# Performance work log

Hardware: AMD Instinct MI355X
Metric: run time of the kernel (lower is better)

## Reference

```python
import jax, jax.numpy as jnp
import numpy as np

B, D_IN, D_HID, D_OUT = 32768, 512, 1024, 2048

def setup_inputs() -> dict:
    key = jax.random.key(0)
    k1, k2, k3, k4 = jax.random.split(key, 4)
    x = jax.random.normal(k1, (B, D_IN), dtype=jnp.float32)
    # linear1 params (torch Linear default-style init, scale approximated)
    l1_w = jax.random.normal(k2, (D_HID, D_IN), dtype=jnp.float32) * (D_IN ** -0.5)
    l1_b = jax.random.normal(k3, (D_HID,), dtype=jnp.float32) * 0.01
    # second linear params: normal(0, hidden^-0.5) weight, zero bias as in source
    weight = jax.random.normal(k4, (D_OUT, D_HID), dtype=jnp.float32) * (D_HID ** -0.5)
    bias = jnp.zeros((D_OUT,), dtype=jnp.float32)
    return {"x": x, "l1_w": l1_w, "l1_b": l1_b, "weight": weight, "bias": bias}

def reference(x, l1_w, l1_b, weight, bias):
    # linear1: [B, D_IN] -> [B, D_HID]
    h = jnp.einsum('bi,hi->bh', x, l1_w) + l1_b
    # fused linear + max epilogue: scores [B, D_OUT] -> max over output dim
    scores = jnp.einsum('bh,oh->bo', h, weight) + bias
    return jnp.max(scores, axis=-1)  # [B]
```

## Files before the change

### kernel.cpp

```cpp
#include <hip/hip_runtime.h>
#include <hip/hip_bf16.h>
#include <stdint.h>

static constexpr int BATCH = 32768;
static constexpr int DIN   = 512;
static constexpr int DHID  = 1024;
static constexpr int DOUT  = 2048;

typedef __bf16 bf16x8 __attribute__((ext_vector_type(8)));
typedef float  f32x4  __attribute__((ext_vector_type(4)));

__device__ __forceinline__ unsigned short f2bf(float f) {
    unsigned int u = __float_as_uint(f);
    u += 0x7FFFu + ((u >> 16) & 1u);
    return (unsigned short)(u >> 16);
}

__device__ __forceinline__ void gload_lds16(const void* g, void* l) {
    __builtin_amdgcn_global_load_lds((__attribute__((address_space(1))) void*)g,
                                     (__attribute__((address_space(3))) void*)l,
                                     16, 0, 0);
}


__global__ __launch_bounds__(256) void prep_kernel(
    const float* __restrict__ w1, const float4* __restrict__ w2f,
    const float4* __restrict__ xf, const float* __restrict__ b1,
    const float* __restrict__ b2,
    unsigned short* __restrict__ w1t, ushort4* __restrict__ w2b,
    ushort4* __restrict__ xb, float* __restrict__ bp) {
    const int blk = blockIdx.x;
    const int t   = threadIdx.x;
    if (blk < 512) {
        __shared__ float tile[32][33];
        const int tileI = blk & 15;
        const int tileH = blk >> 4;
        const int iBase = tileI * 32, hBase = tileH * 32;
        const int col = t & 31, rowq = t >> 5;
#pragma unroll
        for (int p = 0; p < 4; ++p) {
            const int row = p * 8 + rowq;
            tile[row][col] = w1[(size_t)(hBase + row) * DIN + iBase + col];
        }
        __syncthreads();
#pragma unroll
        for (int p = 0; p < 4; ++p) {
            const int row = p * 8 + rowq;
            w1t[(size_t)(iBase + row) * DHID + hBase + col] = f2bf(tile[col][row]);
        }
    } else if (blk < 2560) {
        __shared__ float wsum[4];
        const int o = blk - 512;
        const size_t g = (size_t)o * 256 + t;
        float4 v = w2f[g];
        ushort4 ob;
        ob.x = f2bf(v.x); ob.y = f2bf(v.y); ob.z = f2bf(v.z); ob.w = f2bf(v.w);
        w2b[g] = ob;
        float4 bv = ((const float4*)b1)[t];
        float s = v.x * bv.x + v.y * bv.y + v.z * bv.z + v.w * bv.w;
#pragma unroll
        for (int off = 1; off < 64; off <<= 1) s += __shfl_xor(s, off);
        if ((t & 63) == 0) wsum[t >> 6] = s;
        __syncthreads();
        if (t == 0) bp[o] = wsum[0] + wsum[1] + wsum[2] + wsum[3] + b2[o];
    } else {
        const size_t base = (size_t)(blk - 2560) * 1024 + t;
#pragma unroll
        for (int i = 0; i < 4; ++i) {
            float4 v = xf[base + i * 256];
            ushort4 o;
            o.x = f2bf(v.x); o.y = f2bf(v.y); o.z = f2bf(v.z); o.w = f2bf(v.w);
            xb[base + i * 256] = o;
        }
    }
}

__global__ __launch_bounds__(256) void gemmW_kernel(
    const unsigned short* __restrict__ A,
    const unsigned short* __restrict__ Bw,
    unsigned short* __restrict__ W) {
    constexpr int K = DHID;
    __shared__ __align__(16) unsigned short sA[64 * 128];
    __shared__ __align__(16) unsigned short sB[64 * 128];

    const int tid  = threadIdx.x;
    const int lane = tid & 63;
    const int wid  = tid >> 6;
    const int wr = wid >> 1, wc = wid & 1;
    const int r = lane & 15, q = lane >> 4;
    const int blockN = blockIdx.x * 64;
    const int blockM = blockIdx.y * 64;

    const int chKey = (tid & 15) ^ ((tid >> 4) & 15);
    const size_t aBase = (size_t)(blockM + (tid >> 4)) * K + chKey * 8;
    const size_t bBase = (size_t)(blockN + (tid >> 4)) * K + chKey * 8;

    f32x4 acc[2][2];
#pragma unroll
    for (int mt = 0; mt < 2; ++mt)
#pragma unroll
        for (int nt = 0; nt < 2; ++nt) { f32x4 z = {0.f, 0.f, 0.f, 0.f}; acc[mt][nt] = z; }

    for (int k0 = 0; k0 < K; k0 += 128) {
#pragma unroll
        for (int j = 0; j < 4; ++j) {
            gload_lds16(A  + aBase + (size_t)j * 16 * K + k0, sA + j * 2048 + wid * 512);
            gload_lds16(Bw + bBase + (size_t)j * 16 * K + k0, sB + j * 2048 + wid * 512);
        }
        __syncthreads();
#pragma unroll
        for (int ks = 0; ks < 4; ++ks) {
            const int ch = ((ks << 2) + q) ^ r;
            bf16x8 af[2], bf[2];
#pragma unroll
            for (int mt = 0; mt < 2; ++mt) af[mt] = *(const bf16x8*)&sA[(wr * 32 + mt * 16 + r) * 128 + ch * 8];
#pragma unroll
            for (int nt = 0; nt < 2; ++nt) bf[nt] = *(const bf16x8*)&sB[(wc * 32 + nt * 16 + r) * 128 + ch * 8];
#pragma unroll
            for (int mt = 0; mt < 2; ++mt)
#pragma unroll
                for (int nt = 0; nt < 2; ++nt)
                    acc[mt][nt] = __builtin_amdgcn_mfma_f32_16x16x32_bf16(af[mt], bf[nt], acc[mt][nt], 0, 0, 0);
        }
        __syncthreads();
    }

#pragma unroll
    for (int mt = 0; mt < 2; ++mt) {
        const int row0 = blockM + wr * 32 + mt * 16 + q * 4;
#pragma unroll
        for (int nt = 0; nt < 2; ++nt) {
            const int col = blockN + wc * 32 + nt * 16 + r;
#pragma unroll
            for (int reg = 0; reg < 4; ++reg)
                W[(size_t)(row0 + reg) * DIN + col] = f2bf(acc[mt][nt][reg]);
        }
    }
}

__global__ __launch_bounds__(256, 2) void gemmS_kernel(
    const unsigned short* __restrict__ A,
    const unsigned short* __restrict__ Bw,
    const float* __restrict__ bp,
    float* __restrict__ out) {
    constexpr int K = DIN;
    __shared__ __align__(16) unsigned short lds[40960];

    const int tid  = threadIdx.x;
    const int lane = tid & 63;
    const int wid  = tid >> 6;
    const int r    = lane & 15, q = lane >> 4;

    const int b    = blockIdx.x;
    const int xcd  = b & 7;
    const int j    = b >> 3;
    const int blockM = (xcd * 64 + j) * 64;

    const int sRow = tid >> 2;
    const int swz  = (tid & 3) ^ ((tid >> 3) & 3);
    const unsigned short* aSrc = A  + (size_t)(blockM + sRow) * K + swz * 8;
    const unsigned short* bSrc = Bw + (size_t)sRow * K + swz * 8;

#define STAGE_A(reg, kt) \
    gload_lds16(aSrc + (kt) * 32, lds + (reg) * 2048 + wid * 512)
#define STAGE_B(bT, reg, kt) do {                                               \
    gload_lds16((bT) + (size_t)(0 * 64) * K + (kt) * 32,                        \
                lds + 8192 + (reg) * 8192 + 0 * 2048 + wid * 512);              \
    gload_lds16((bT) + (size_t)(1 * 64) * K + (kt) * 32,                        \
                lds + 8192 + (reg) * 8192 + 1 * 2048 + wid * 512);              \
    gload_lds16((bT) + (size_t)(2 * 64) * K + (kt) * 32,                        \
                lds + 8192 + (reg) * 8192 + 2 * 2048 + wid * 512);              \
    gload_lds16((bT) + (size_t)(3 * 64) * K + (kt) * 32,                        \
                lds + 8192 + (reg) * 8192 + 3 * 2048 + wid * 512);              \
} while (0)

    const int fOff = (q ^ ((r >> 1) & 3)) * 8;
    const unsigned short* ldsAf = lds + r * 32 + fOff;
    const unsigned short* ldsBf = lds + 8192 + (wid * 64 + r) * 32 + fOff;

    f32x4 acc[4][4];
#pragma unroll
    for (int mt = 0; mt < 4; ++mt)
#pragma unroll
        for (int nt = 0; nt < 4; ++nt) { f32x4 z = {0.f, 0.f, 0.f, 0.f}; acc[mt][nt] = z; }
    float mx[4][4];
#pragma unroll
    for (int mt = 0; mt < 4; ++mt)
#pragma unroll
        for (int rg = 0; rg < 4; ++rg) mx[mt][rg] = -INFINITY;
    bf16x8 af[4], bfr[4];
    float bvc[4], bvn[4];

#define RD(reg) do {                                                            \
    const unsigned short* pa_ = ldsAf + (reg) * 2048;                           \
    af[0] = *(const bf16x8*)(pa_);                                              \
    af[1] = *(const bf16x8*)(pa_ + 512);                                        \
    af[2] = *(const bf16x8*)(pa_ + 1024);                                       \
    af[3] = *(const bf16x8*)(pa_ + 1536);                                       \
    const unsigned short* pb_ = ldsBf + (reg) * 8192;                           \
    bfr[0] = *(const bf16x8*)(pb_);                                             \
    bfr[1] = *(const bf16x8*)(pb_ + 512);                                       \
    bfr[2] = *(const bf16x8*)(pb_ + 1024);                                      \
    bfr[3] = *(const bf16x8*)(pb_ + 1536);                                      \
} while (0)
#define MM() do {                                                               \
    __builtin_amdgcn_s_setprio(1);                                              \
    _Pragma("unroll") for (int m_ = 0; m_ < 4; ++m_)                            \
    _Pragma("unroll") for (int n_ = 0; n_ < 4; ++n_)                            \
        acc[m_][n_] = __builtin_amdgcn_mfma_f32_16x16x32_bf16(                  \
            af[m_], bfr[n_], acc[m_][n_], 0, 0, 0);                             \
    __builtin_amdgcn_s_setprio(0);                                              \
} while (0)
#define BAR()   __builtin_amdgcn_s_barrier()
#define LGKM0() asm volatile("s_waitcnt lgkmcnt(0)" ::: "memory")
#define VMC(n)  asm volatile("s_waitcnt vmcnt(" #n ")" ::: "memory")

#define PH(reg, sreg, skt, bT) do {                                             \
    RD(reg);                                                                    \
    STAGE_A(sreg, skt); STAGE_B(bT, sreg, skt);                                 \
    VMC(10); LGKM0(); MM(); BAR();                                              \
} while (0)
#define PH15(reg, sreg, skt, bT, bOff) do {                                     \
    RD(reg);                                                                    \
    bvn[0] = bp[(bOff) + wid * 64 + 0 * 16 + r];                                \
    bvn[1] = bp[(bOff) + wid * 64 + 1 * 16 + r];                                \
    bvn[2] = bp[(bOff) + wid * 64 + 2 * 16 + r];                                \
    bvn[3] = bp[(bOff) + wid * 64 + 3 * 16 + r];                                \
    __builtin_amdgcn_sched_barrier(0);                                          \
    STAGE_A(sreg, skt); STAGE_B(bT, sreg, skt);                                 \
    VMC(10); LGKM0(); MM(); BAR();                                              \
} while (0)

#define FOLD() do {                                                             \
    _Pragma("unroll") for (int mt_ = 0; mt_ < 4; ++mt_)                         \
    _Pragma("unroll") for (int rg_ = 0; rg_ < 4; ++rg_) {                       \
        float v_ = fmaxf(fmaxf(acc[mt_][0][rg_] + bvc[0],                       \
                               acc[mt_][1][rg_] + bvc[1]),                      \
                         fmaxf(acc[mt_][2][rg_] + bvc[2],                       \
                               acc[mt_][3][rg_] + bvc[3]));                     \
        mx[mt_][rg_] = fmaxf(mx[mt_][rg_], v_);                                 \
    }                                                                           \
} while (0)
#define ACC_ZERO() do {                                                         \
    _Pragma("unroll") for (int mt_ = 0; mt_ < 4; ++mt_)                         \
    _Pragma("unroll") for (int nt_ = 0; nt_ < 4; ++nt_) {                       \
        f32x4 z_ = {0.f, 0.f, 0.f, 0.f}; acc[mt_][nt_] = z_;                    \
    }                                                                           \
} while (0)

#pragma unroll
    for (int nt = 0; nt < 4; ++nt) bvc[nt] = bp[wid * 64 + nt * 16 + r];
    VMC(0);

    STAGE_A(0, 0); STAGE_B(bSrc, 0, 0);
    STAGE_A(1, 1); STAGE_B(bSrc, 1, 1);
    STAGE_A(2, 2); STAGE_B(bSrc, 2, 2);
    VMC(10);
    BAR();

#pragma unroll 1
    for (int t = 0; t < 7; ++t) {
        const unsigned short* bT  = bSrc + (size_t)t * 256 * K;
        const unsigned short* bTn = bT + (size_t)256 * K;
        PH(0, 3, 3, bT);
        PH(1, 0, 4, bT);
        PH(2, 1, 5, bT);
        PH(3, 2, 6, bT);
        PH(0, 3, 7, bT);
        PH(1, 0, 8, bT);
        PH(2, 1, 9, bT);
        PH(3, 2, 10, bT);
        PH(0, 3, 11, bT);
        PH(1, 0, 12, bT);
        PH(2, 1, 13, bT);
        PH(3, 2, 14, bT);
        PH(0, 3, 15, bT);
        PH(1, 0, 0, bTn);
        PH(2, 1, 1, bTn);
        PH15(3, 2, 2, bTn, (t + 1) * 256);
        FOLD();
        ACC_ZERO();
#pragma unroll
        for (int nt = 0; nt < 4; ++nt) bvc[nt] = bvn[nt];
    }
    {
        const unsigned short* bT = bSrc + (size_t)7 * 256 * K;
        PH(0, 3, 3, bT);
        PH(1, 0, 4, bT);
        PH(2, 1, 5, bT);
        PH(3, 2, 6, bT);
        PH(0, 3, 7, bT);
        PH(1, 0, 8, bT);
        PH(2, 1, 9, bT);
        PH(3, 2, 10, bT);
        PH(0, 3, 11, bT);
        PH(1, 0, 12, bT);
        PH(2, 1, 13, bT);
        PH(3, 2, 14, bT);
        PH(0, 3, 15, bT);
        RD(1); VMC(5); LGKM0(); MM(); BAR();
        RD(2); VMC(0); LGKM0(); MM(); BAR();
        RD(3); LGKM0(); MM();
        FOLD();
    }

#undef STAGE_A
#undef STAGE_B
#undef RD
#undef MM
#undef BAR
#undef LGKM0
#undef VMC
#undef PH
#undef PH15
#undef FOLD
#undef ACC_ZERO

    __syncthreads();
    float* smax = (float*)lds;
#pragma unroll
    for (int mt = 0; mt < 4; ++mt) {
#pragma unroll
        for (int rg = 0; rg < 4; ++rg) {
            float v = mx[mt][rg];
#pragma unroll
            for (int off = 1; off < 16; off <<= 1)
                v = fmaxf(v, __shfl_xor(v, off));
            if (r == 0) smax[(mt * 16 + q * 4 + rg) * 4 + wid] = v;
        }
    }
    __syncthreads();
    if (tid < 64) {
        const float* p = smax + tid * 4;
        out[blockM + tid] = fmaxf(fmaxf(p[0], p[1]), fmaxf(p[2], p[3]));
    }
}

extern "C" void kernel_launch(void* const* d_in, const int* in_sizes, int n_in,
                              void* d_out, int out_size, void* d_ws, size_t ws_size,
                              hipStream_t stream) {
    const float* x   = (const float*)d_in[0];
    const float* l1w = (const float*)d_in[1];
    const float* l1b = (const float*)d_in[2];
    const float* w2  = (const float*)d_in[3];
    const float* b2  = (const float*)d_in[4];
    float* out = (float*)d_out;

    char* ws = (char*)d_ws;
    unsigned short* w1t = (unsigned short*)(ws);
    unsigned short* w2b = (unsigned short*)(ws + 1048576);
    unsigned short* Wb  = (unsigned short*)(ws + 5242880);
    float* bp           = (float*)(ws + 7340032);
    unsigned short* xb  = (unsigned short*)(ws + 7348224);

    prep_kernel<<<6656, 256, 0, stream>>>(
        l1w, (const float4*)w2, (const float4*)x, l1b, b2,
        w1t, (ushort4*)w2b, (ushort4*)xb, bp);

    gemmW_kernel<<<dim3(DIN / 64, DOUT / 64), 256, 0, stream>>>(w2b, w1t, Wb);

    gemmS_kernel<<<512, 256, 0, stream>>>(xb, Wb, bp, out);
}
```

Baseline: 203.0 us.

## Keep full A row-block resident in LDS and stream B fragments directly from global

The main GEMM+max kernel now uses 512-thread blocks covering 128 rows, split across 2x4 waves. The whole K=512 slice of A (128x512 bf16) is staged into LDS once, and B fragments are loaded straight from global/L2 into registers with even/odd double buffering. After the first 256-column tile this removes the per-step LDS staging of B and the per-phase barriers. The cost is a large LDS footprint (~136KB) that limits occupancy to one block per CU, plus B reads that depend on L2 latency being hidden by register prefetch.

New measurement: 239.6 us. +18.0%, slower.

```diff
diff --git a/kernel.cpp b/kernel.cpp
--- a/kernel.cpp
+++ b/kernel.cpp
@@ -138,45 +138,40 @@
     }
 }
 
-__global__ __launch_bounds__(256, 2) void gemmS_kernel(
+__global__ __launch_bounds__(512, 2) void gemmS_kernel(
     const unsigned short* __restrict__ A,
     const unsigned short* __restrict__ Bw,
     const float* __restrict__ bp,
     float* __restrict__ out) {
-    constexpr int K = DIN;
-    __shared__ __align__(16) unsigned short lds[40960];
+    __shared__ __align__(16) unsigned short lds[69632];
 
     const int tid  = threadIdx.x;
     const int lane = tid & 63;
     const int wid  = tid >> 6;
+    const int wr   = wid >> 2;
+    const int wc   = wid & 3;
     const int r    = lane & 15, q = lane >> 4;
 
     const int b    = blockIdx.x;
     const int xcd  = b & 7;
     const int j    = b >> 3;
-    const int blockM = (xcd * 64 + j) * 64;
+    const int blockM = (xcd * 32 + j) * 128;
 
     const int sRow = tid >> 2;
     const int swz  = (tid & 3) ^ ((tid >> 3) & 3);
-    const unsigned short* aSrc = A  + (size_t)(blockM + sRow) * K + swz * 8;
-    const unsigned short* bSrc = Bw + (size_t)sRow * K + swz * 8;
-
-#define STAGE_A(reg, kt) \
-    gload_lds16(aSrc + (kt) * 32, lds + (reg) * 2048 + wid * 512)
-#define STAGE_B(bT, reg, kt) do {                                               \
-    gload_lds16((bT) + (size_t)(0 * 64) * K + (kt) * 32,                        \
-                lds + 8192 + (reg) * 8192 + 0 * 2048 + wid * 512);              \
-    gload_lds16((bT) + (size_t)(1 * 64) * K + (kt) * 32,                        \
-                lds + 8192 + (reg) * 8192 + 1 * 2048 + wid * 512);              \
-    gload_lds16((bT) + (size_t)(2 * 64) * K + (kt) * 32,                        \
-                lds + 8192 + (reg) * 8192 + 2 * 2048 + wid * 512);              \
-    gload_lds16((bT) + (size_t)(3 * 64) * K + (kt) * 32,                        \
-                lds + 8192 + (reg) * 8192 + 3 * 2048 + wid * 512);              \
-} while (0)
+    const unsigned short* aSrc = A + (size_t)(blockM + sRow) * DIN + swz * 8;
+    float* biasLds = (float*)(lds + 65536);
+
+#define STAGE_A(s) \
+    gload_lds16(aSrc + (s) * 32, lds + (s) * 4096 + wid * 512)
 
     const int fOff = (q ^ ((r >> 1) & 3)) * 8;
-    const unsigned short* ldsAf = lds + r * 32 + fOff;
-    const unsigned short* ldsBf = lds + 8192 + (wid * 64 + r) * 32 + fOff;
+    const unsigned short* ldsAf = lds + (wr * 64 + r) * 32 + fOff;
+
+    const unsigned short* bT0 = Bw + (size_t)(wc * 64 + 0 * 16 + r) * DIN + q * 8;
+    const unsigned short* bT1 = Bw + (size_t)(wc * 64 + 1 * 16 + r) * DIN + q * 8;
+    const unsigned short* bT2 = Bw + (size_t)(wc * 64 + 2 * 16 + r) * DIN + q * 8;
+    const unsigned short* bT3 = Bw + (size_t)(wc * 64 + 3 * 16 + r) * DIN + q * 8;
 
     f32x4 acc[4][4];
 #pragma unroll
@@ -188,48 +183,48 @@
     for (int mt = 0; mt < 4; ++mt)
 #pragma unroll
         for (int rg = 0; rg < 4; ++rg) mx[mt][rg] = -INFINITY;
-    bf16x8 af[4], bfr[4];
-    float bvc[4], bvn[4];
-
-#define RD(reg) do {                                                            \
-    const unsigned short* pa_ = ldsAf + (reg) * 2048;                           \
+    bf16x8 af[4], bfrE[4], bfrO[4];
+    float bvc[4];
+
+#define RD_A(s) do {                                                            \
+    const unsigned short* pa_ = ldsAf + (s) * 4096;                             \
     af[0] = *(const bf16x8*)(pa_);                                              \
     af[1] = *(const bf16x8*)(pa_ + 512);                                        \
     af[2] = *(const bf16x8*)(pa_ + 1024);                                       \
     af[3] = *(const bf16x8*)(pa_ + 1536);                                       \
-    const unsigned short* pb_ = ldsBf + (reg) * 8192;                           \
-    bfr[0] = *(const bf16x8*)(pb_);                                             \
-    bfr[1] = *(const bf16x8*)(pb_ + 512);                                       \
-    bfr[2] = *(const bf16x8*)(pb_ + 1024);                                      \
-    bfr[3] = *(const bf16x8*)(pb_ + 1536);                                      \
-} while (0)
-#define MM() do {                                                               \
+} while (0)
+#define BPREF_E(soff) do {                                                      \
+    bfrE[0] = *(const bf16x8*)(bT0 + (soff));                                   \
+    bfrE[1] = *(const bf16x8*)(bT1 + (soff));                                   \
+    bfrE[2] = *(const bf16x8*)(bT2 + (soff));                                   \
+    bfrE[3] = *(const bf16x8*)(bT3 + (soff));                                   \
+} while (0)
+#define BPREF_O(soff) do {                                                      \
+    bfrO[0] = *(const bf16x8*)(bT0 + (soff));                                   \
+    bfrO[1] = *(const bf16x8*)(bT1 + (soff));                                   \
+    bfrO[2] = *(const bf16x8*)(bT2 + (soff));                                   \
+    bfrO[3] = *(const bf16x8*)(bT3 + (soff));                                   \
+} while (0)
+#define MM_E() do {                                                             \
     __builtin_amdgcn_s_setprio(1);                                              \
     _Pragma("unroll") for (int m_ = 0; m_ < 4; ++m_)                            \
     _Pragma("unroll") for (int n_ = 0; n_ < 4; ++n_)                            \
         acc[m_][n_] = __builtin_amdgcn_mfma_f32_16x16x32_bf16(                  \
-            af[m_], bfr[n_], acc[m_][n_], 0, 0, 0);                             \
+            af[m_], bfrE[n_], acc[m_][n_], 0, 0, 0);                            \
     __builtin_amdgcn_s_setprio(0);                                              \
 } while (0)
+#define MM_O() do {                                                             \
+    __builtin_amdgcn_s_setprio(1);                                              \
+    _Pragma("unroll") for (int m_ = 0; m_ < 4; ++m_)                            \
+    _Pragma("unroll") for (int n_ = 0; n_ < 4; ++n_)                            \
+        acc[m_][n_] = __builtin_amdgcn_mfma_f32_16x16x32_bf16(                  \
+            af[m_], bfrO[n_], acc[m_][n_], 0, 0, 0);                            \
+    __builtin_amdgcn_s_setprio(0);                                              \
+} while (0)
 #define BAR()   __builtin_amdgcn_s_barrier()
+#define SB0()   __builtin_amdgcn_sched_barrier(0)
 #define LGKM0() asm volatile("s_waitcnt lgkmcnt(0)" ::: "memory")
 #define VMC(n)  asm volatile("s_waitcnt vmcnt(" #n ")" ::: "memory")
-
-#define PH(reg, sreg, skt, bT) do {                                             \
-    RD(reg);                                                                    \
-    STAGE_A(sreg, skt); STAGE_B(bT, sreg, skt);                                 \
-    VMC(10); LGKM0(); MM(); BAR();                                              \
-} while (0)
-#define PH15(reg, sreg, skt, bT, bOff) do {                                     \
-    RD(reg);                                                                    \
-    bvn[0] = bp[(bOff) + wid * 64 + 0 * 16 + r];                                \
-    bvn[1] = bp[(bOff) + wid * 64 + 1 * 16 + r];                                \
-    bvn[2] = bp[(bOff) + wid * 64 + 2 * 16 + r];                                \
-    bvn[3] = bp[(bOff) + wid * 64 + 3 * 16 + r];                                \
-    __builtin_amdgcn_sched_barrier(0);                                          \
-    STAGE_A(sreg, skt); STAGE_B(bT, sreg, skt);                                 \
-    VMC(10); LGKM0(); MM(); BAR();                                              \
-} while (0)
 
 #define FOLD() do {                                                             \
     _Pragma("unroll") for (int mt_ = 0; mt_ < 4; ++mt_)                         \
@@ -248,71 +243,103 @@
     }                                                                           \
 } while (0)
 
-#pragma unroll
-    for (int nt = 0; nt < 4; ++nt) bvc[nt] = bp[wid * 64 + nt * 16 + r];
-    VMC(0);
-
-    STAGE_A(0, 0); STAGE_B(bSrc, 0, 0);
-    STAGE_A(1, 1); STAGE_B(bSrc, 1, 1);
-    STAGE_A(2, 2); STAGE_B(bSrc, 2, 2);
-    VMC(10);
+    {
+        float4 bb = ((const float4*)bp)[tid];
+        ((float4*)biasLds)[tid] = bb;
+    }
+    LGKM0();
+
+    BPREF_E(0);
+    STAGE_A(0); STAGE_A(1); STAGE_A(2);
+    VMC(2);
     BAR();
 
+#pragma unroll
+    for (int nt = 0; nt < 4; ++nt) bvc[nt] = biasLds[wc * 64 + nt * 16 + r];
+
+#define PH0S(s, PREF, MM_) do {                                                 \
+    RD_A(s); PREF((s + 1) * 32); STAGE_A((s) + 3);                              \
+    VMC(6); LGKM0(); SB0(); MM_(); BAR();                                       \
+} while (0)
+    PH0S(0,  BPREF_O, MM_E);
+    PH0S(1,  BPREF_E, MM_O);
+    PH0S(2,  BPREF_O, MM_E);
+    PH0S(3,  BPREF_E, MM_O);
+    PH0S(4,  BPREF_O, MM_E);
+    PH0S(5,  BPREF_E, MM_O);
+    PH0S(6,  BPREF_O, MM_E);
+    PH0S(7,  BPREF_E, MM_O);
+    PH0S(8,  BPREF_O, MM_E);
+    PH0S(9,  BPREF_E, MM_O);
+    PH0S(10, BPREF_O, MM_E);
+    PH0S(11, BPREF_E, MM_O);
+    PH0S(12, BPREF_O, MM_E);
+    RD_A(13); BPREF_E(14 * 32); VMC(4); LGKM0(); SB0(); MM_O(); BAR();
+    RD_A(14); BPREF_O(15 * 32); VMC(4); LGKM0(); SB0(); MM_E(); BAR();
+    RD_A(15); BPREF_E(131072); VMC(4); LGKM0(); SB0(); MM_O(); BAR();
+    FOLD(); ACC_ZERO();
+#pragma unroll
+    for (int nt = 0; nt < 4; ++nt) bvc[nt] = biasLds[256 + wc * 64 + nt * 16 + r];
+    bT0 += 131072; bT1 += 131072; bT2 += 131072; bT3 += 131072;
+#undef PH0S
+
+#define PHS(s, PREF, MM_) do {                                                  \
+    RD_A(s); PREF((s + 1) * 32);                                                \
+    VMC(4); LGKM0(); SB0(); MM_();                                              \
+} while (0)
 #pragma unroll 1
-    for (int t = 0; t < 7; ++t) {
-        const unsigned short* bT  = bSrc + (size_t)t * 256 * K;
-        const unsigned short* bTn = bT + (size_t)256 * K;
-        PH(0, 3, 3, bT);
-        PH(1, 0, 4, bT);
-        PH(2, 1, 5, bT);
-        PH(3, 2, 6, bT);
-        PH(0, 3, 7, bT);
-        PH(1, 0, 8, bT);
-        PH(2, 1, 9, bT);
-        PH(3, 2, 10, bT);
-        PH(0, 3, 11, bT);
-        PH(1, 0, 12, bT);
-        PH(2, 1, 13, bT);
-        PH(3, 2, 14, bT);
-        PH(0, 3, 15, bT);
-        PH(1, 0, 0, bTn);
-        PH(2, 1, 1, bTn);
-        PH15(3, 2, 2, bTn, (t + 1) * 256);
-        FOLD();
-        ACC_ZERO();
-#pragma unroll
-        for (int nt = 0; nt < 4; ++nt) bvc[nt] = bvn[nt];
-    }
-    {
-        const unsigned short* bT = bSrc + (size_t)7 * 256 * K;
-        PH(0, 3, 3, bT);
-        PH(1, 0, 4, bT);
-        PH(2, 1, 5, bT);
-        PH(3, 2, 6, bT);
-        PH(0, 3, 7, bT);
-        PH(1, 0, 8, bT);
-        PH(2, 1, 9, bT);
-        PH(3, 2, 10, bT);
-        PH(0, 3, 11, bT);
-        PH(1, 0, 12, bT);
-        PH(2, 1, 13, bT);
-        PH(3, 2, 14, bT);
-        PH(0, 3, 15, bT);
-        RD(1); VMC(5); LGKM0(); MM(); BAR();
-        RD(2); VMC(0); LGKM0(); MM(); BAR();
-        RD(3); LGKM0(); MM();
-        FOLD();
-    }
+    for (int t = 1; t < 7; ++t) {
+        PHS(0,  BPREF_O, MM_E);
+        PHS(1,  BPREF_E, MM_O);
+        PHS(2,  BPREF_O, MM_E);
+        PHS(3,  BPREF_E, MM_O);
+        PHS(4,  BPREF_O, MM_E);
+        PHS(5,  BPREF_E, MM_O);
+        PHS(6,  BPREF_O, MM_E);
+        PHS(7,  BPREF_E, MM_O);
+        PHS(8,  BPREF_O, MM_E);
+        PHS(9,  BPREF_E, MM_O);
+        PHS(10, BPREF_O, MM_E);
+        PHS(11, BPREF_E, MM_O);
+        PHS(12, BPREF_O, MM_E);
+        PHS(13, BPREF_E, MM_O);
+        PHS(14, BPREF_O, MM_E);
+        RD_A(15); BPREF_E(131072); VMC(4); LGKM0(); SB0(); MM_O();
+        FOLD(); ACC_ZERO();
+#pragma unroll
+        for (int nt = 0; nt < 4; ++nt)
+            bvc[nt] = biasLds[(t + 1) * 256 + wc * 64 + nt * 16 + r];
+        bT0 += 131072; bT1 += 131072; bT2 += 131072; bT3 += 131072;
+    }
+    PHS(0,  BPREF_O, MM_E);
+    PHS(1,  BPREF_E, MM_O);
+    PHS(2,  BPREF_O, MM_E);
+    PHS(3,  BPREF_E, MM_O);
+    PHS(4,  BPREF_O, MM_E);
+    PHS(5,  BPREF_E, MM_O);
+    PHS(6,  BPREF_O, MM_E);
+    PHS(7,  BPREF_E, MM_O);
+    PHS(8,  BPREF_O, MM_E);
+    PHS(9,  BPREF_E, MM_O);
+    PHS(10, BPREF_O, MM_E);
+    PHS(11, BPREF_E, MM_O);
+    PHS(12, BPREF_O, MM_E);
+    PHS(13, BPREF_E, MM_O);
+    PHS(14, BPREF_O, MM_E);
+    RD_A(15); VMC(0); LGKM0(); SB0(); MM_O();
+    FOLD();
+#undef PHS
 
 #undef STAGE_A
-#undef STAGE_B
-#undef RD
-#undef MM
+#undef RD_A
+#undef BPREF_E
+#undef BPREF_O
+#undef MM_E
+#undef MM_O
 #undef BAR
+#undef SB0
 #undef LGKM0
 #undef VMC
-#undef PH
-#undef PH15
 #undef FOLD
 #undef ACC_ZERO
 
@@ -326,11 +353,11 @@
 #pragma unroll
             for (int off = 1; off < 16; off <<= 1)
                 v = fmaxf(v, __shfl_xor(v, off));
-            if (r == 0) smax[(mt * 16 + q * 4 + rg) * 4 + wid] = v;
+            if (r == 0) smax[(wr * 64 + mt * 16 + q * 4 + rg) * 4 + wc] = v;
         }
     }
     __syncthreads();
-    if (tid < 64) {
+    if (tid < 128) {
         const float* p = smax + tid * 4;
         out[blockM + tid] = fmaxf(fmaxf(p[0], p[1]), fmaxf(p[2], p[3]));
     }
@@ -359,5 +386,5 @@
 
     gemmW_kernel<<<dim3(DIN / 64, DOUT / 64), 256, 0, stream>>>(w2b, w1t, Wb);
 
-    gemmS_kernel<<<512, 256, 0, stream>>>(xb, Wb, bp, out);
-}
+    gemmS_kernel<<<256, 512, 0, stream>>>(xb, Wb, bp, out);
+}
```
